# Kernel optimization log

Hardware: AMD Instinct MI355X
Metric: run time of the kernel (lower is better)

The kernel has to match this reference:

```python
import jax, jax.numpy as jnp
import numpy as np

N_ATOMS = 5000
N_PAIRS = 160000
N_STRUCT = 16
N_SPECIES = 4
L_MAX = 2
K = 128            # k_max per l (rectangular)
N_BASIS = 8        # radial basis size
RAD_HIDDEN = 32    # radial MLP hidden
CUTOFF = 5.0
MSG_SCALE = 0.1767767   # ~1/sqrt(avg_degree)
INIT_SCALE = 0.2        # hypers['initial_scaling']


def _orthogonal(key, n):
    m = jax.random.normal(key, (n, n))
    q, r = jnp.linalg.qr(m)
    return q * jnp.sign(jnp.diag(r))[None, :]


def setup_inputs() -> dict:
    key = jax.random.key(0)
    ks = jax.random.split(key, 24)
    positions = jax.random.normal(ks[0], (N_ATOMS, 3)) * 1.5
    cells = jax.random.normal(ks[1], (N_STRUCT, 3, 3)) * 0.5
    species = jax.random.randint(ks[2], (N_ATOMS,), 0, N_SPECIES)
    cell_shifts = jax.random.randint(ks[3], (N_PAIRS, 3), 0, 3).astype(jnp.int32)
    center_indices = jax.random.randint(ks[4], (N_PAIRS,), 0, N_ATOMS)
    neighbor_indices = jax.random.randint(ks[5], (N_PAIRS,), 0, N_ATOMS)
    structure_pairs = jax.random.randint(ks[6], (N_PAIRS,), 0, N_STRUCT)
    s = lambda k, sh, f: jax.random.normal(k, sh) * f
    params = dict(
        embed=s(ks[7], (N_SPECIES, K), 1.0),
        rad_w1=s(ks[8], (N_BASIS, RAD_HIDDEN), 0.3), rad_b1=jnp.zeros((RAD_HIDDEN,)),
        rad_w2=s(ks[9], (RAD_HIDDEN, (L_MAX + 1) * K), 0.3), rad_b2=jnp.zeros(((L_MAX + 1) * K,)),
        erad_w1=s(ks[10], (N_BASIS, RAD_HIDDEN), 0.3), erad_b1=jnp.zeros((RAD_HIDDEN,)),
        erad_w2=s(ks[11], (RAD_HIDDEN, (L_MAX + 1) * K), 0.3), erad_b2=jnp.zeros(((L_MAX + 1) * K,)),
        mix_a=s(ks[12], (L_MAX + 1, K), 0.5),
        emix_a=s(ks[13], (L_MAX + 1, K), 0.5),
        head_w1=s(ks[14], (K, K), 0.1), head_b1=jnp.zeros((K,)),
        head_w2=s(ks[15], (K, K), 0.1), head_b2=jnp.zeros((K,)),
        last_w=s(ks[16], (K, 1), 0.1), last_b=jnp.zeros((1,)),
        U2=_orthogonal(ks[20], 9),  # orthogonal CG change-of-basis, U @ U.T = I
    )
    return dict(positions=positions, cells=cells, species=species,
                cell_shifts=cell_shifts, center_indices=center_indices,
                neighbor_indices=neighbor_indices, structure_pairs=structure_pairs,
                **params)


def _sph(unit):
    # real spherical harmonics up to l=2, inputs are unit vectors [P,3]
    x, y, z = unit[:, 0], unit[:, 1], unit[:, 2]
    sh0 = jnp.ones_like(x)[:, None]
    sh1 = jnp.stack([y, z, x], axis=1)
    c = jnp.sqrt(3.0)
    sh2 = jnp.stack([c * x * y, c * y * z, 0.5 * (3 * z * z - 1.0),
                     c * x * z, 0.5 * c * (x * x - y * y)], axis=1)
    return [sh0, sh1, sh2]


def _radial(d, w1, b1, w2, b2):
    # Gaussian radial basis * smooth cutoff -> MLP -> per-l K channels
    centers = jnp.linspace(0.0, CUTOFF, N_BASIS)
    rb = jnp.exp(-((d[:, None] - centers[None, :]) ** 2) / (2.0 * 0.5 ** 2))
    fcut = jnp.where(d < CUTOFF, 0.5 * (jnp.cos(jnp.pi * d / CUTOFF) + 1.0), 0.0)
    h = jax.nn.silu((rb * fcut[:, None]) @ w1 + b1)
    return (h @ w2 + b2).reshape(-1, L_MAX + 1, K)  # [P, l, K]


def _uncouple(f, l, U2):
    # coupled [N, 2l+1, K] -> uncoupled matrix [N, 3, 3, K] (padded_l = 2)
    if l == 0:
        return f[:, :, None, :]
    n, _, k = f.shape
    vec = jnp.zeros((n, 9, k), f.dtype)
    off = 1 if l == 1 else 4
    vec = vec.at[:, off:off + 2 * l + 1, :].set(f)
    unc = jnp.einsum('qp,nqk->npk', U2, vec)  # U2.T @ vec
    return unc.reshape(n, 3, 3, k)


def _couple(unc, l, U2):
    if l == 0:
        return unc[:, :, 0, :]
    n, k = unc.shape[0], unc.shape[-1]
    vec = jnp.einsum('pq,nqk->npk', U2, unc.reshape(n, 9, k))
    off = 1 if l == 1 else 4
    return vec[:, off:off + 2 * l + 1, :]


def _cg_iterate(feats, U2, mix):
    # CG tensor product iteration in the uncoupled (matrix) basis:
    # matrix product A@A is equivariant under A -> D A D^T
    out = []
    for l, f in enumerate(feats):
        A = _uncouple(f, l, U2)
        C = jnp.einsum('nimk,nmjk->nijk', A, A)
        out.append(_couple(A + C * mix[l][None, None, None, :], l, U2))
    return out


def _forward(positions, cells, embed, rad_w1, rad_b1, rad_w2, rad_b2,
             erad_w1, erad_b1, erad_w2, erad_b2, mix_a, emix_a,
             head_w1, head_b1, head_w2, head_b2, last_w, last_b, U2,
             species, cell_shifts, center_indices, neighbor_indices, structure_pairs):
    # pair vectors with PBC shifts
    shifts = cell_shifts.astype(positions.dtype) - 1.0  # -> {-1,0,1}
    vec = positions[neighbor_indices] - positions[center_indices] \
        + jnp.einsum('pi,pij->pj', shifts, cells[structure_pairs])
    d = jnp.sqrt(jnp.sum(vec * vec, axis=1) + 1e-12)
    unit = vec / d[:, None]
    sh = [s * INIT_SCALE for s in _sph(unit)]
    Rk = _radial(d, rad_w1, rad_b1, rad_w2, rad_b2)      # [P, 3, K]
    emb_n = embed[species][neighbor_indices]             # [P, K]

    # invariant message passing: sh_l x radial x neighbor embedding, scatter to centers
    feats = []
    for l in range(L_MAX + 1):
        msg = sh[l][:, :, None] * Rk[:, l, None, :] * emb_n[:, None, :]
        feats.append(jax.ops.segment_sum(msg, center_indices, num_segments=N_ATOMS) * MSG_SCALE)

    feats = _cg_iterate(feats, U2, mix_a)

    # equivariant message passing layer
    Rke = _radial(d, erad_w1, erad_b1, erad_w2, erad_b2)
    inv_n = feats[0][neighbor_indices, 0, :]             # [P, K] invariant part
    new = []
    for l in range(L_MAX + 1):
        g = feats[l][neighbor_indices]                   # [P, 2l+1, K]
        msg = sh[l][:, :, None] * Rke[:, l, None, :] * inv_n[:, None, :] \
            + Rke[:, 0, None, :] * g
        new.append(feats[l] + jax.ops.segment_sum(msg, center_indices, num_segments=N_ATOMS) * MSG_SCALE)

    feats = _cg_iterate(new, U2, emix_a)

    # scalar (l=0) MLP head + last linear layer
    h = feats[0][:, 0, :]
    h = jax.nn.silu(h @ head_w1 + head_b1)
    h = jax.nn.silu(h @ head_w2 + head_b2)
    return h @ last_w + last_b  # [N_ATOMS, 1]


def reference(positions, cells, species, cell_shifts, center_indices,
              neighbor_indices, structure_pairs, embed, rad_w1, rad_b1, rad_w2,
              rad_b2, erad_w1, erad_b1, erad_w2, erad_b2, mix_a, emix_a,
              head_w1, head_b1, head_w2, head_b2, last_w, last_b, U2):
    return _forward(positions, cells, embed, rad_w1, rad_b1, rad_w2, rad_b2,
                    erad_w1, erad_b1, erad_w2, erad_b2, mix_a, emix_a,
                    head_w1, head_b1, head_w2, head_b2, last_w, last_b, U2,
                    species, cell_shifts, center_indices, neighbor_indices,
                    structure_pairs)
```

## Files before the change

kernel.cpp:

```cpp
#include <hip/hip_runtime.h>

constexpr int   kAtoms  = 5000;
constexpr int   kPairs  = 160000;
constexpr int   KD      = 128;
constexpr int   NB      = 8;
constexpr int   RH      = 32;
constexpr float kCutoff = 5.0f;
constexpr float kPi     = 3.14159265358979323846f;
constexpr float C1 = 0.2f * 0.1767767f;
constexpr float C2 = 1.2f * 0.1767767f;
constexpr int   WCH = 32;

__device__ __forceinline__ float silu(float x) { return x / (1.0f + __expf(-x)); }
__device__ __forceinline__ void wave_fence() { __builtin_amdgcn_wave_barrier(); }


__global__ __launch_bounds__(256) void hist_kernel(
    const int* __restrict__ ctr, int* __restrict__ cnt)
{
    int p = blockIdx.x * 256 + threadIdx.x;
    atomicAdd(cnt + ctr[p], 1);
}

__global__ __launch_bounds__(1024) void scan_kernel(
    const int* __restrict__ cnt, int* __restrict__ off, int* __restrict__ cur)
{
    __shared__ int s_part[1024];
    const int CH = 5;
    int t = threadIdx.x;
    int base = t * CH;
    int loc[CH];
    int run = 0;
    #pragma unroll
    for (int i = 0; i < CH; i++) {
        int idx = base + i;
        int v = (idx < kAtoms) ? cnt[idx] : 0;
        loc[i] = run;
        run += v;
    }
    s_part[t] = run;
    __syncthreads();
    for (int st = 1; st < 1024; st <<= 1) {
        int v = (t >= st) ? s_part[t - st] : 0;
        __syncthreads();
        s_part[t] += v;
        __syncthreads();
    }
    int excl = (t > 0) ? s_part[t - 1] : 0;
    #pragma unroll
    for (int i = 0; i < CH; i++) {
        int idx = base + i;
        if (idx < kAtoms) { off[idx] = excl + loc[i]; cur[idx] = excl + loc[i]; }
    }
    if (t == 1023) off[kAtoms] = s_part[1023];
}

__global__ __launch_bounds__(256) void build_kernel(
    const float* __restrict__ pos, const float* __restrict__ cells,
    const int* __restrict__ species, const int* __restrict__ shifts,
    const int* __restrict__ ctr, const int* __restrict__ nbr,
    const int* __restrict__ spair,
    int* __restrict__ cur, int* __restrict__ nbrs_s, int* __restrict__ specs_s,
    float* __restrict__ rbf_s)
{
    int p = blockIdx.x * 256 + threadIdx.x;
    int ci = ctr[p], ni = nbr[p], sp = spair[p];
    float s0 = (float)shifts[p * 3 + 0] - 1.0f;
    float s1 = (float)shifts[p * 3 + 1] - 1.0f;
    float s2 = (float)shifts[p * 3 + 2] - 1.0f;
    const float* C = cells + sp * 9;
    float vx = pos[ni * 3 + 0] - pos[ci * 3 + 0] + s0 * C[0] + s1 * C[3] + s2 * C[6];
    float vy = pos[ni * 3 + 1] - pos[ci * 3 + 1] + s0 * C[1] + s1 * C[4] + s2 * C[7];
    float vz = pos[ni * 3 + 2] - pos[ci * 3 + 2] + s0 * C[2] + s1 * C[5] + s2 * C[8];
    float d = sqrtf(vx * vx + vy * vy + vz * vz + 1e-12f);
    float fcut = (d < kCutoff) ? 0.5f * (__cosf(kPi * d / kCutoff) + 1.0f) : 0.0f;

    int slot = atomicAdd(cur + ci, 1);
    nbrs_s[slot]  = ni;
    specs_s[slot] = species[ni];

    float r[NB];
    #pragma unroll
    for (int i = 0; i < NB; i++) {
        float tt = d - (kCutoff / (NB - 1)) * (float)i;
        r[i] = __expf(-2.0f * tt * tt) * fcut;
    }
    float4* dst = (float4*)(rbf_s + (size_t)slot * NB);
    dst[0] = make_float4(r[0], r[1], r[2], r[3]);
    dst[1] = make_float4(r[4], r[5], r[6], r[7]);
}

__global__ __launch_bounds__(256) void f0_kernel(
    const float* __restrict__ rbf_s, const int* __restrict__ specs_s,
    const int* __restrict__ off,
    const float* __restrict__ embed,
    const float* __restrict__ w1, const float* __restrict__ b1,
    const float* __restrict__ w2, const float* __restrict__ b2,
    const float* __restrict__ mix,
    float* __restrict__ G0)
{
    __shared__ float s_w1[NB][RH];
    __shared__ float s_b1v[RH];
    __shared__ float s_H[4][2][4][RH];
    __shared__ float s_Hc[4][4][RH];
    __shared__ float s_n[4][2][4];

    int t = threadIdx.x, w = t >> 6, lane = t & 63;
    for (int idx = t; idx < NB * RH; idx += 256)
        s_w1[idx >> 5][idx & 31] = w1[idx];
    if (t < RH) s_b1v[t] = b1[t];
    __syncthreads();

    int a = blockIdx.x * 4 + w;
    int start = off[a], m = off[a + 1] - start;

    int g = lane >> 5, j = lane & 31;
    float H0 = 0, H1 = 0, H2 = 0, H3 = 0;
    int   n0 = 0, n1 = 0, n2 = 0, n3 = 0;
    float b1j = s_b1v[j];
    for (int pr = g; pr < m; pr += 2) {
        const float* rb = rbf_s + (size_t)(start + pr) * NB;
        float acc = b1j;
        #pragma unroll
        for (int i = 0; i < NB; i++) acc += rb[i] * s_w1[i][j];
        float h = silu(acc);
        int s = specs_s[start + pr];
        H0 += (s == 0) ? h : 0.0f;  H1 += (s == 1) ? h : 0.0f;
        H2 += (s == 2) ? h : 0.0f;  H3 += (s == 3) ? h : 0.0f;
        n0 += (s == 0); n1 += (s == 1); n2 += (s == 2); n3 += (s == 3);
    }
    s_H[w][g][0][j] = H0; s_H[w][g][1][j] = H1;
    s_H[w][g][2][j] = H2; s_H[w][g][3][j] = H3;
    if (j == 0) {
        s_n[w][g][0] = (float)n0; s_n[w][g][1] = (float)n1;
        s_n[w][g][2] = (float)n2; s_n[w][g][3] = (float)n3;
    }
    wave_fence();
    #pragma unroll
    for (int e = lane; e < 4 * RH; e += 64) {
        int s = e >> 5, jj = e & 31;
        s_Hc[w][s][jj] = s_H[w][0][s][jj] + s_H[w][1][s][jj];
    }
    wave_fence();
    float nc0 = s_n[w][0][0] + s_n[w][1][0];
    float nc1 = s_n[w][0][1] + s_n[w][1][1];
    float nc2 = s_n[w][0][2] + s_n[w][1][2];
    float nc3 = s_n[w][0][3] + s_n[w][1][3];

    #pragma unroll
    for (int half = 0; half < 2; half++) {
        int k = lane + 64 * half;
        float e0 = embed[0 * KD + k], e1 = embed[1 * KD + k];
        float e2 = embed[2 * KD + k], e3 = embed[3 * KD + k];
        float P0 = 0, P1 = 0, P2 = 0, P3 = 0;
        #pragma unroll
        for (int jq = 0; jq < RH / 4; jq++) {
            float4 h0 = *(const float4*)&s_Hc[w][0][4 * jq];
            float4 h1 = *(const float4*)&s_Hc[w][1][4 * jq];
            float4 h2 = *(const float4*)&s_Hc[w][2][4 * jq];
            float4 h3 = *(const float4*)&s_Hc[w][3][4 * jq];
            float wa = w2[(4 * jq + 0) * (3 * KD) + k];
            float wb = w2[(4 * jq + 1) * (3 * KD) + k];
            float wc = w2[(4 * jq + 2) * (3 * KD) + k];
            float wd = w2[(4 * jq + 3) * (3 * KD) + k];
            P0 += h0.x * wa + h0.y * wb + h0.z * wc + h0.w * wd;
            P1 += h1.x * wa + h1.y * wb + h1.z * wc + h1.w * wd;
            P2 += h2.x * wa + h2.y * wb + h2.z * wc + h2.w * wd;
            P3 += h3.x * wa + h3.y * wb + h3.z * wc + h3.w * wd;
        }
        float F = b2[k] * (nc0 * e0 + nc1 * e1 + nc2 * e2 + nc3 * e3)
                + e0 * P0 + e1 * P1 + e2 * P2 + e3 * P3;
        float F0v = C1 * F;
        G0[(size_t)a * KD + k] = F0v + F0v * F0v * mix[k];
    }
}

__global__ __launch_bounds__(256) void d0_kernel(
    const float* __restrict__ rbf_s, const int* __restrict__ nbrs_s,
    const int* __restrict__ off,
    const float* __restrict__ w1, const float* __restrict__ b1,
    const float* __restrict__ w2, const float* __restrict__ b2,
    const float* __restrict__ emix,
    const float* __restrict__ G0,
    float* __restrict__ V)
{
    __shared__ float s_w1[NB][RH];
    __shared__ float s_b1v[RH];
    __shared__ float s_h[4][WCH][RH];
    __shared__ int   s_nbr[4][WCH];

    int t = threadIdx.x, w = t >> 6, lane = t & 63;
    for (int idx = t; idx < NB * RH; idx += 256)
        s_w1[idx >> 5][idx & 31] = w1[idx];
    if (t < RH) s_b1v[t] = b1[t];
    __syncthreads();

    int a = blockIdx.x * 4 + w;
    int start = off[a], end = off[a + 1];
    int k0 = lane, k1 = lane + 64;

    float w2c0[RH], w2c1[RH];
    #pragma unroll
    for (int j = 0; j < RH; j++) {
        w2c0[j] = w2[j * (3 * KD) + k0];
        w2c1[j] = w2[j * (3 * KD) + k1];
    }
    float b2k0 = b2[k0], b2k1 = b2[k1];

    int g = lane >> 5, j = lane & 31;
    float b1j = s_b1v[j];

    float Dacc0 = 0.0f, Dacc1 = 0.0f;
    for (int c = start; c < end; c += WCH) {
        int m = min(WCH, end - c);
        wave_fence();
        for (int pr = g; pr < m; pr += 2) {
            const float* rb = rbf_s + (size_t)(c + pr) * NB;
            float acc = b1j;
            #pragma unroll
            for (int i = 0; i < NB; i++) acc += rb[i] * s_w1[i][j];
            s_h[w][pr][j] = silu(acc);
        }
        if (lane < m) s_nbr[w][lane] = nbrs_s[c + lane];
        wave_fence();
        #pragma unroll 2
        for (int i = 0; i < m; i++) {
            const float* gbase = G0 + (size_t)s_nbr[w][i] * KD;
            float gv0 = gbase[k0];
            float gv1 = gbase[k1];
            float R0 = b2k0, R1 = b2k1;
            #pragma unroll
            for (int jq = 0; jq < RH / 4; jq++) {
                float4 h4 = *(const float4*)&s_h[w][i][4 * jq];
                R0 += h4.x * w2c0[4 * jq + 0] + h4.y * w2c0[4 * jq + 1]
                    + h4.z * w2c0[4 * jq + 2] + h4.w * w2c0[4 * jq + 3];
                R1 += h4.x * w2c1[4 * jq + 0] + h4.y * w2c1[4 * jq + 1]
                    + h4.z * w2c1[4 * jq + 2] + h4.w * w2c1[4 * jq + 3];
            }
            Dacc0 += R0 * gv0;
            Dacc1 += R1 * gv1;
        }
    }
    float n0 = G0[(size_t)a * KD + k0] + C2 * Dacc0;
    float n1 = G0[(size_t)a * KD + k1] + C2 * Dacc1;
    V[(size_t)a * KD + k0] = n0 + n0 * n0 * emix[k0];
    V[(size_t)a * KD + k1] = n1 + n1 * n1 * emix[k1];
}

__global__ __launch_bounds__(128) void head_kernel(
    const float* __restrict__ V,
    const float* __restrict__ w1, const float* __restrict__ b1,
    const float* __restrict__ w2, const float* __restrict__ b2,
    const float* __restrict__ lw, const float* __restrict__ lb,
    float* __restrict__ out)
{
    __shared__ float s_a[8][KD];
    __shared__ float s_b[8][KD];
    int j = threadIdx.x;
    int abase = blockIdx.x * 8;

    #pragma unroll
    for (int a = 0; a < 8; a++) {
        int ga = abase + a;
        s_a[a][j] = (ga < kAtoms) ? V[(size_t)ga * KD + j] : 0.0f;
    }
    __syncthreads();

    float acc[8];
    float bj = b1[j];
    #pragma unroll
    for (int a = 0; a < 8; a++) acc[a] = bj;
    for (int kk = 0; kk < KD; kk += 4) {
        float wa = w1[(kk + 0) * KD + j], wb = w1[(kk + 1) * KD + j];
        float wc = w1[(kk + 2) * KD + j], wd = w1[(kk + 3) * KD + j];
        #pragma unroll
        for (int a = 0; a < 8; a++) {
            float4 v = *(const float4*)&s_a[a][kk];
            acc[a] += v.x * wa + v.y * wb + v.z * wc + v.w * wd;
        }
    }
    #pragma unroll
    for (int a = 0; a < 8; a++) s_b[a][j] = silu(acc[a]);
    __syncthreads();

    float b2j = b2[j];
    #pragma unroll
    for (int a = 0; a < 8; a++) acc[a] = b2j;
    for (int kk = 0; kk < KD; kk += 4) {
        float wa = w2[(kk + 0) * KD + j], wb = w2[(kk + 1) * KD + j];
        float wc = w2[(kk + 2) * KD + j], wd = w2[(kk + 3) * KD + j];
        #pragma unroll
        for (int a = 0; a < 8; a++) {
            float4 v = *(const float4*)&s_b[a][kk];
            acc[a] += v.x * wa + v.y * wb + v.z * wc + v.w * wd;
        }
    }
    float lwj = lw[j];
    __syncthreads();
    #pragma unroll
    for (int a = 0; a < 8; a++) s_a[a][j] = silu(acc[a]) * lwj;
    __syncthreads();
    for (int s = 64; s > 0; s >>= 1) {
        if (j < s) {
            #pragma unroll
            for (int a = 0; a < 8; a++) s_a[a][j] += s_a[a][j + s];
        }
        __syncthreads();
    }
    if (j < 8) {
        int ga = abase + j;
        if (ga < kAtoms) out[ga] = s_a[j][0] + lb[0];
    }
}

extern "C" void kernel_launch(void* const* d_in, const int* in_sizes, int n_in,
                              void* d_out, int out_size, void* d_ws, size_t ws_size,
                              hipStream_t stream) {
    const float* positions = (const float*)d_in[0];
    const float* cells     = (const float*)d_in[1];
    const int*   species   = (const int*)d_in[2];
    const int*   shifts    = (const int*)d_in[3];
    const int*   ctr       = (const int*)d_in[4];
    const int*   nbr       = (const int*)d_in[5];
    const int*   spair     = (const int*)d_in[6];
    const float* embed     = (const float*)d_in[7];
    const float* rad_w1    = (const float*)d_in[8];
    const float* rad_b1    = (const float*)d_in[9];
    const float* rad_w2    = (const float*)d_in[10];
    const float* rad_b2    = (const float*)d_in[11];
    const float* erad_w1   = (const float*)d_in[12];
    const float* erad_b1   = (const float*)d_in[13];
    const float* erad_w2   = (const float*)d_in[14];
    const float* erad_b2   = (const float*)d_in[15];
    const float* mix_a     = (const float*)d_in[16];
    const float* emix_a    = (const float*)d_in[17];
    const float* head_w1   = (const float*)d_in[18];
    const float* head_b1   = (const float*)d_in[19];
    const float* head_w2   = (const float*)d_in[20];
    const float* head_b2   = (const float*)d_in[21];
    const float* last_w    = (const float*)d_in[22];
    const float* last_b    = (const float*)d_in[23];

    float* rbf_s = (float*)d_ws;
    float* G0    = rbf_s + (size_t)kPairs * NB;
    float* V     = G0    + (size_t)kAtoms * KD;
    int*   cnt   = (int*)(V + (size_t)kAtoms * KD);
    int*   off   = cnt + kAtoms;
    int*   cur   = off + kAtoms + 1;
    int*   nbrs  = cur + kAtoms;
    int*   specs = nbrs + kPairs;

    hipMemsetAsync(cnt, 0, kAtoms * sizeof(int), stream);

    hist_kernel<<<kPairs / 256, 256, 0, stream>>>(ctr, cnt);
    scan_kernel<<<1, 1024, 0, stream>>>(cnt, off, cur);
    build_kernel<<<kPairs / 256, 256, 0, stream>>>(
        positions, cells, species, shifts, ctr, nbr, spair,
        cur, nbrs, specs, rbf_s);

    f0_kernel<<<kAtoms / 4, 256, 0, stream>>>(
        rbf_s, specs, off, embed, rad_w1, rad_b1, rad_w2, rad_b2,
        mix_a, G0);

    d0_kernel<<<kAtoms / 4, 256, 0, stream>>>(
        rbf_s, nbrs, off, erad_w1, erad_b1, erad_w2, erad_b2,
        emix_a, G0, V);

    head_kernel<<<(kAtoms + 7) / 8, 128, 0, stream>>>(
        V, head_w1, head_b1, head_w2, head_b2, last_w, last_b,
        (float*)d_out);
}
```

Measured before the change: 225.4 us.

## Precompute edge hidden layer in build kernel and fuse message pass with head MLP

```diff
diff --git a/kernel.cpp b/kernel.cpp
--- a/kernel.cpp
+++ b/kernel.cpp
@@ -9,7 +9,6 @@
 constexpr float kPi     = 3.14159265358979323846f;
 constexpr float C1 = 0.2f * 0.1767767f;
 constexpr float C2 = 1.2f * 0.1767767f;
-constexpr int   WCH = 32;
 
 __device__ __forceinline__ float silu(float x) { return x / (1.0f + __expf(-x)); }
 __device__ __forceinline__ void wave_fence() { __builtin_amdgcn_wave_barrier(); }
@@ -60,8 +59,9 @@
     const int* __restrict__ species, const int* __restrict__ shifts,
     const int* __restrict__ ctr, const int* __restrict__ nbr,
     const int* __restrict__ spair,
+    const float* __restrict__ ew1, const float* __restrict__ eb1,
     int* __restrict__ cur, int* __restrict__ nbrs_s, int* __restrict__ specs_s,
-    float* __restrict__ rbf_s)
+    float* __restrict__ rbf_s, float* __restrict__ hbuf)
 {
     int p = blockIdx.x * 256 + threadIdx.x;
     int ci = ctr[p], ni = nbr[p], sp = spair[p];
@@ -85,9 +85,24 @@
         float tt = d - (kCutoff / (NB - 1)) * (float)i;
         r[i] = __expf(-2.0f * tt * tt) * fcut;
     }
-    float4* dst = (float4*)(rbf_s + (size_t)slot * NB);
-    dst[0] = make_float4(r[0], r[1], r[2], r[3]);
-    dst[1] = make_float4(r[4], r[5], r[6], r[7]);
+    float4* rdst = (float4*)(rbf_s + (size_t)slot * NB);
+    rdst[0] = make_float4(r[0], r[1], r[2], r[3]);
+    rdst[1] = make_float4(r[4], r[5], r[6], r[7]);
+
+    float* hdst = hbuf + (size_t)slot * RH;
+    #pragma unroll
+    for (int jq = 0; jq < RH / 4; jq++) {
+        float4 hv; float* pv = (float*)&hv;
+        #pragma unroll
+        for (int u = 0; u < 4; u++) {
+            int j = 4 * jq + u;
+            float acc = eb1[j];
+            #pragma unroll
+            for (int i = 0; i < NB; i++) acc += r[i] * ew1[i * RH + j];
+            pv[u] = silu(acc);
+        }
+        *(float4*)(hdst + 4 * jq) = hv;
+    }
 }
 
 __global__ __launch_bounds__(256) void f0_kernel(
@@ -175,142 +190,97 @@
     }
 }
 
-__global__ __launch_bounds__(256) void d0_kernel(
-    const float* __restrict__ rbf_s, const int* __restrict__ nbrs_s,
+__global__ void d0head_kernel(
+    const float* __restrict__ hbuf, const int* __restrict__ nbrs_s,
     const int* __restrict__ off,
-    const float* __restrict__ w1, const float* __restrict__ b1,
     const float* __restrict__ w2, const float* __restrict__ b2,
     const float* __restrict__ emix,
     const float* __restrict__ G0,
-    float* __restrict__ V)
-{
-    __shared__ float s_w1[NB][RH];
-    __shared__ float s_b1v[RH];
-    __shared__ float s_h[4][WCH][RH];
-    __shared__ int   s_nbr[4][WCH];
-
-    int t = threadIdx.x, w = t >> 6, lane = t & 63;
-    for (int idx = t; idx < NB * RH; idx += 256)
-        s_w1[idx >> 5][idx & 31] = w1[idx];
-    if (t < RH) s_b1v[t] = b1[t];
-    __syncthreads();
-
-    int a = blockIdx.x * 4 + w;
-    int start = off[a], end = off[a + 1];
-    int k0 = lane, k1 = lane + 64;
-
-    float w2c0[RH], w2c1[RH];
-    #pragma unroll
-    for (int j = 0; j < RH; j++) {
-        w2c0[j] = w2[j * (3 * KD) + k0];
-        w2c1[j] = w2[j * (3 * KD) + k1];
-    }
-    float b2k0 = b2[k0], b2k1 = b2[k1];
-
-    int g = lane >> 5, j = lane & 31;
-    float b1j = s_b1v[j];
-
-    float Dacc0 = 0.0f, Dacc1 = 0.0f;
-    for (int c = start; c < end; c += WCH) {
-        int m = min(WCH, end - c);
-        wave_fence();
-        for (int pr = g; pr < m; pr += 2) {
-            const float* rb = rbf_s + (size_t)(c + pr) * NB;
-            float acc = b1j;
-            #pragma unroll
-            for (int i = 0; i < NB; i++) acc += rb[i] * s_w1[i][j];
-            s_h[w][pr][j] = silu(acc);
-        }
-        if (lane < m) s_nbr[w][lane] = nbrs_s[c + lane];
-        wave_fence();
-        #pragma unroll 2
-        for (int i = 0; i < m; i++) {
-            const float* gbase = G0 + (size_t)s_nbr[w][i] * KD;
-            float gv0 = gbase[k0];
-            float gv1 = gbase[k1];
-            float R0 = b2k0, R1 = b2k1;
-            #pragma unroll
-            for (int jq = 0; jq < RH / 4; jq++) {
-                float4 h4 = *(const float4*)&s_h[w][i][4 * jq];
-                R0 += h4.x * w2c0[4 * jq + 0] + h4.y * w2c0[4 * jq + 1]
-                    + h4.z * w2c0[4 * jq + 2] + h4.w * w2c0[4 * jq + 3];
-                R1 += h4.x * w2c1[4 * jq + 0] + h4.y * w2c1[4 * jq + 1]
-                    + h4.z * w2c1[4 * jq + 2] + h4.w * w2c1[4 * jq + 3];
-            }
-            Dacc0 += R0 * gv0;
-            Dacc1 += R1 * gv1;
-        }
-    }
-    float n0 = G0[(size_t)a * KD + k0] + C2 * Dacc0;
-    float n1 = G0[(size_t)a * KD + k1] + C2 * Dacc1;
-    V[(size_t)a * KD + k0] = n0 + n0 * n0 * emix[k0];
-    V[(size_t)a * KD + k1] = n1 + n1 * n1 * emix[k1];
-}
-
-__global__ __launch_bounds__(128) void head_kernel(
-    const float* __restrict__ V,
-    const float* __restrict__ w1, const float* __restrict__ b1,
-    const float* __restrict__ w2, const float* __restrict__ b2,
+    const float* __restrict__ hw1, const float* __restrict__ hb1,
+    const float* __restrict__ hw2, const float* __restrict__ hb2,
     const float* __restrict__ lw, const float* __restrict__ lb,
     float* __restrict__ out)
 {
-    __shared__ float s_a[8][KD];
-    __shared__ float s_b[8][KD];
-    int j = threadIdx.x;
-    int abase = blockIdx.x * 8;
-
-    #pragma unroll
-    for (int a = 0; a < 8; a++) {
-        int ga = abase + a;
-        s_a[a][j] = (ga < kAtoms) ? V[(size_t)ga * KD + j] : 0.0f;
-    }
-    __syncthreads();
-
-    float acc[8];
-    float bj = b1[j];
-    #pragma unroll
-    for (int a = 0; a < 8; a++) acc[a] = bj;
+    __shared__ float s_v[4][KD];
+    __shared__ float s_m[4][KD];
+
+    int t = threadIdx.x, w = t >> 6, lane = t & 63;
+    int a = blockIdx.x * 4 + w;
+    int start = __builtin_amdgcn_readfirstlane(off[a]);
+    int end   = __builtin_amdgcn_readfirstlane(off[a + 1]);
+
+    int k0 = 2 * lane, k1 = 2 * lane + 1;
+    float w2c0[RH], w2c1[RH];
+    #pragma unroll
+    for (int j = 0; j < RH; j++) {
+        float2 wv = *(const float2*)&w2[j * (3 * KD) + k0];
+        w2c0[j] = wv.x; w2c1[j] = wv.y;
+    }
+    float b2k0 = b2[k0], b2k1 = b2[k1];
+
+    float D0 = 0.0f, D1 = 0.0f;
+    for (int i = start; i < end; i++) {
+        int nb = __builtin_amdgcn_readfirstlane(nbrs_s[i]);
+        const float* h = hbuf + (size_t)i * RH;
+        float2 gv = *(const float2*)(G0 + (size_t)nb * KD + k0);
+        float4 h4[RH / 4];
+        #pragma unroll
+        for (int q = 0; q < RH / 4; q++) h4[q] = *(const float4*)(h + 4 * q);
+        float R0 = b2k0, R1 = b2k1;
+        #pragma unroll
+        for (int q = 0; q < RH / 4; q++) {
+            R0 += h4[q].x * w2c0[4*q+0] + h4[q].y * w2c0[4*q+1]
+                + h4[q].z * w2c0[4*q+2] + h4[q].w * w2c0[4*q+3];
+            R1 += h4[q].x * w2c1[4*q+0] + h4[q].y * w2c1[4*q+1]
+                + h4[q].z * w2c1[4*q+2] + h4[q].w * w2c1[4*q+3];
+        }
+        D0 += R0 * gv.x;
+        D1 += R1 * gv.y;
+    }
+    {
+        float2 ga = *(const float2*)(G0 + (size_t)a * KD + k0);
+        float q0 = ga.x + C2 * D0, q1 = ga.y + C2 * D1;
+        s_v[w][k0] = q0 + q0 * q0 * emix[k0];
+        s_v[w][k1] = q1 + q1 * q1 * emix[k1];
+    }
+    __syncthreads();
+
+    int j = t & 127, grp = t >> 7;
+    int a0 = grp * 2, a1 = grp * 2 + 1;
+    float acc0 = hb1[j], acc1 = acc0;
     for (int kk = 0; kk < KD; kk += 4) {
-        float wa = w1[(kk + 0) * KD + j], wb = w1[(kk + 1) * KD + j];
-        float wc = w1[(kk + 2) * KD + j], wd = w1[(kk + 3) * KD + j];
-        #pragma unroll
-        for (int a = 0; a < 8; a++) {
-            float4 v = *(const float4*)&s_a[a][kk];
-            acc[a] += v.x * wa + v.y * wb + v.z * wc + v.w * wd;
-        }
-    }
-    #pragma unroll
-    for (int a = 0; a < 8; a++) s_b[a][j] = silu(acc[a]);
-    __syncthreads();
-
-    float b2j = b2[j];
-    #pragma unroll
-    for (int a = 0; a < 8; a++) acc[a] = b2j;
+        float wa = hw1[(kk+0)*KD+j], wb = hw1[(kk+1)*KD+j];
+        float wc = hw1[(kk+2)*KD+j], wd = hw1[(kk+3)*KD+j];
+        float4 v0 = *(const float4*)&s_v[a0][kk];
+        float4 v1 = *(const float4*)&s_v[a1][kk];
+        acc0 += v0.x*wa + v0.y*wb + v0.z*wc + v0.w*wd;
+        acc1 += v1.x*wa + v1.y*wb + v1.z*wc + v1.w*wd;
+    }
+    s_m[a0][j] = silu(acc0);
+    s_m[a1][j] = silu(acc1);
+    __syncthreads();
+    acc0 = hb2[j]; acc1 = acc0;
     for (int kk = 0; kk < KD; kk += 4) {
-        float wa = w2[(kk + 0) * KD + j], wb = w2[(kk + 1) * KD + j];
-        float wc = w2[(kk + 2) * KD + j], wd = w2[(kk + 3) * KD + j];
-        #pragma unroll
-        for (int a = 0; a < 8; a++) {
-            float4 v = *(const float4*)&s_b[a][kk];
-            acc[a] += v.x * wa + v.y * wb + v.z * wc + v.w * wd;
-        }
+        float wa = hw2[(kk+0)*KD+j], wb = hw2[(kk+1)*KD+j];
+        float wc = hw2[(kk+2)*KD+j], wd = hw2[(kk+3)*KD+j];
+        float4 v0 = *(const float4*)&s_m[a0][kk];
+        float4 v1 = *(const float4*)&s_m[a1][kk];
+        acc0 += v0.x*wa + v0.y*wb + v0.z*wc + v0.w*wd;
+        acc1 += v1.x*wa + v1.y*wb + v1.z*wc + v1.w*wd;
     }
     float lwj = lw[j];
     __syncthreads();
-    #pragma unroll
-    for (int a = 0; a < 8; a++) s_a[a][j] = silu(acc[a]) * lwj;
+    s_v[a0][j] = silu(acc0) * lwj;
+    s_v[a1][j] = silu(acc1) * lwj;
     __syncthreads();
     for (int s = 64; s > 0; s >>= 1) {
         if (j < s) {
-            #pragma unroll
-            for (int a = 0; a < 8; a++) s_a[a][j] += s_a[a][j + s];
+            s_v[a0][j] += s_v[a0][j + s];
+            s_v[a1][j] += s_v[a1][j + s];
         }
         __syncthreads();
     }
-    if (j < 8) {
-        int ga = abase + j;
-        if (ga < kAtoms) out[ga] = s_a[j][0] + lb[0];
-    }
+    if (t < 4) out[blockIdx.x * 4 + t] = s_v[t][0] + lb[0];
 }
 
 extern "C" void kernel_launch(void* const* d_in, const int* in_sizes, int n_in,
@@ -342,9 +312,9 @@
     const float* last_b    = (const float*)d_in[23];
 
     float* rbf_s = (float*)d_ws;
-    float* G0    = rbf_s + (size_t)kPairs * NB;
-    float* V     = G0    + (size_t)kAtoms * KD;
-    int*   cnt   = (int*)(V + (size_t)kAtoms * KD);
+    float* hbuf  = rbf_s + (size_t)kPairs * NB;
+    float* G0    = hbuf + (size_t)kPairs * RH;
+    int*   cnt   = (int*)(G0 + (size_t)kAtoms * KD);
     int*   off   = cnt + kAtoms;
     int*   cur   = off + kAtoms + 1;
     int*   nbrs  = cur + kAtoms;
@@ -356,17 +326,14 @@
     scan_kernel<<<1, 1024, 0, stream>>>(cnt, off, cur);
     build_kernel<<<kPairs / 256, 256, 0, stream>>>(
         positions, cells, species, shifts, ctr, nbr, spair,
-        cur, nbrs, specs, rbf_s);
+        erad_w1, erad_b1, cur, nbrs, specs, rbf_s, hbuf);
 
     f0_kernel<<<kAtoms / 4, 256, 0, stream>>>(
         rbf_s, specs, off, embed, rad_w1, rad_b1, rad_w2, rad_b2,
         mix_a, G0);
 
-    d0_kernel<<<kAtoms / 4, 256, 0, stream>>>(
-        rbf_s, nbrs, off, erad_w1, erad_b1, erad_w2, erad_b2,
-        emix_a, G0, V);
-
-    head_kernel<<<(kAtoms + 7) / 8, 128, 0, stream>>>(
-        V, head_w1, head_b1, head_w2, head_b2, last_w, last_b,
+    d0head_kernel<<<kAtoms / 4, 256, 0, stream>>>(
+        hbuf, nbrs, off, erad_w2, erad_b2, emix_a, G0,
+        head_w1, head_b1, head_w2, head_b2, last_w, last_b,
         (float*)d_out);
 }
```

New measurement: 233.0 us. +3.4%, slower.
